# Kernel tuning notes

Hardware: AMD Instinct MI355X
Metric: run time of the kernel (lower is better)

The kernel has to match this reference:

```python
import jax, jax.numpy as jnp
import numpy as np

IN, HID, OUT, PHEAD = 128, 256, 256, 64
N0, E0, ND0, E1, ND1 = 1048576, 2097152, 131072, 131072, 8192

def setup_inputs() -> dict:
    key = jax.random.key(0)
    ks = jax.random.split(key, 12)
    x = jax.random.normal(ks[0], (N0, IN), dtype=jnp.float32)
    src0 = jax.random.randint(ks[1], (E0,), 0, N0)
    dst0 = jax.random.randint(ks[2], (E0,), 0, ND0)
    src1 = jax.random.randint(ks[3], (E1,), 0, ND0)
    dst1 = jax.random.randint(ks[4], (E1,), 0, ND1)
    s1 = 1.0 / np.sqrt(IN); s2 = 1.0 / np.sqrt(HID); s3 = 1.0 / np.sqrt(OUT)
    W1 = jax.random.uniform(ks[5], (HID, IN), jnp.float32, -s1, s1)
    b1 = jax.random.uniform(ks[6], (HID,), jnp.float32, -s1, s1)
    W2 = jax.random.uniform(ks[7], (OUT, HID), jnp.float32, -s2, s2)
    b2 = jax.random.uniform(ks[8], (OUT,), jnp.float32, -s2, s2)
    Wh = jax.random.uniform(ks[9], (PHEAD, OUT), jnp.float32, -s3, s3)
    bh = jax.random.uniform(ks[10], (PHEAD,), jnp.float32, -s3, s3)
    return {"x": x, "src0": src0, "dst0": dst0, "src1": src1, "dst1": dst1,
            "W1": W1, "b1": b1, "W2": W2, "b2": b2, "Wh": Wh, "bh": bh,
            "n_dst0": ND0, "n_dst1": ND1, "task_index": 0}

def sage_gcn(feat_src, feat_dst, src, dst, n_dst, W, b):
    # DGL SAGEConv aggregator_type='gcn': (sum_neighbors + self) / (deg + 1), then fc_neigh
    neigh = jax.ops.segment_sum(feat_src[src], dst, num_segments=n_dst)
    deg = jax.ops.segment_sum(jnp.ones((src.shape[0],), feat_src.dtype), dst, num_segments=n_dst)
    h = (neigh + feat_dst) / (deg + 1.0)[:, None]
    return h @ W.T + b

def reference(x, src0, dst0, src1, dst1, W1, b1, W2, b2, Wh, bh, n_dst0, n_dst1, task_index):
    h_dst = x[:n_dst0]
    h = jax.nn.relu(sage_gcn(x, h_dst, src0, dst0, n_dst0, W1, b1))
    h_dst = h[:n_dst1]
    h = jax.nn.relu(sage_gcn(h, h_dst, src1, dst1, n_dst1, W2, b2))
    if task_index == -1:
        return h
    return h @ Wh.T + bh
```

## Files before the change

kernel.cpp:

```cpp
#include <hip/hip_runtime.h>


#define GEMM_BM 64
#define GEMM_BN 64
#define GEMM_BK 32

__global__ __launch_bounds__(256) void hist_kernel(const int* __restrict__ dst,
                                                   int* __restrict__ count, int E) {
    int e = blockIdx.x * 256 + threadIdx.x;
    if (e >= E) return;
    atomicAdd(&count[dst[e]], 1);
}

__global__ __launch_bounds__(256) void block_sum_kernel(const int* __restrict__ count,
                                                        int* __restrict__ bsum) {
    __shared__ int sdata[256];
    int t = threadIdx.x;
    int i = blockIdx.x * 1024 + t * 4;
    int s = count[i] + count[i + 1] + count[i + 2] + count[i + 3];
    sdata[t] = s;
    __syncthreads();
    for (int off = 128; off > 0; off >>= 1) {
        if (t < off) sdata[t] += sdata[t + off];
        __syncthreads();
    }
    if (t == 0) bsum[blockIdx.x] = sdata[0];
}

__global__ __launch_bounds__(256) void scan_small_kernel(const int* __restrict__ bsum,
                                                         int* __restrict__ boff, int nb) {
    __shared__ int sdata[256];
    int t = threadIdx.x;
    int v = (t < nb) ? bsum[t] : 0;
    sdata[t] = v;
    __syncthreads();
    int val = v;
    for (int off = 1; off < 256; off <<= 1) {
        int x = (t >= off) ? sdata[t - off] : 0;
        __syncthreads();
        val += x;
        sdata[t] = val;
        __syncthreads();
    }
    if (t < nb) boff[t] = val - v;
}

__global__ __launch_bounds__(256) void scan_final_kernel(const int* __restrict__ count,
                                                         const int* __restrict__ boff,
                                                         int* __restrict__ row_start,
                                                         int* __restrict__ cursor) {
    __shared__ int sdata[256];
    int t = threadIdx.x;
    int base_i = blockIdx.x * 1024 + t * 4;
    int c0 = count[base_i], c1 = count[base_i + 1], c2 = count[base_i + 2], c3 = count[base_i + 3];
    int local = c0 + c1 + c2 + c3;
    sdata[t] = local;
    __syncthreads();
    int val = local;
    for (int off = 1; off < 256; off <<= 1) {
        int x = (t >= off) ? sdata[t - off] : 0;
        __syncthreads();
        val += x;
        sdata[t] = val;
        __syncthreads();
    }
    int base = boff[blockIdx.x] + (val - local);
    int r0 = base, r1 = r0 + c0, r2 = r1 + c1, r3 = r2 + c2;
    row_start[base_i] = r0; row_start[base_i + 1] = r1;
    row_start[base_i + 2] = r2; row_start[base_i + 3] = r3;
    cursor[base_i] = r0; cursor[base_i + 1] = r1;
    cursor[base_i + 2] = r2; cursor[base_i + 3] = r3;
}

__global__ __launch_bounds__(256) void fill_kernel(const int* __restrict__ src,
                                                   const int* __restrict__ dst,
                                                   int* __restrict__ cursor,
                                                   int* __restrict__ edge_src, int E) {
    int e = blockIdx.x * 256 + threadIdx.x;
    if (e >= E) return;
    int d = dst[e];
    int p = atomicAdd(&cursor[d], 1);
    edge_src[p] = src[e];
}

template<int RF> struct VecSel;
template<> struct VecSel<2> { using V = float2; };
template<> struct VecSel<4> { using V = float4; };

template<int RF>
__global__ __launch_bounds__(256) void agg_kernel(const float* __restrict__ feat,
                                                  const float* __restrict__ selff,
                                                  const int* __restrict__ row_start,
                                                  const int* __restrict__ count,
                                                  const int* __restrict__ edge_src,
                                                  float* __restrict__ neigh,
                                                  float* __restrict__ deg, int ND) {
    using V = typename VecSel<RF>::V;
    int w = (blockIdx.x * 256 + threadIdx.x) >> 6;
    int lane = threadIdx.x & 63;
    if (w >= ND) return;
    const int K = 64 * RF;
    size_t lo = (size_t)w * K + (size_t)lane * RF;
    V acc = *(const V*)(selff + lo);
    const int rs = row_start[w];
    const int cnt = count[w];

    for (int base = 0; base < cnt; base += 64) {
        const int rem = min(cnt - base, 64);
        const int idx = edge_src[rs + base + min(lane, rem - 1)];

        for (int jj = 0; jj < rem; jj += 8) {
            int s[8];
            float m[8];
            #pragma unroll
            for (int k = 0; k < 8; ++k) {
                int j = jj + k;
                s[k] = __shfl(idx, min(j, rem - 1));
                m[k] = (j < rem) ? 1.0f : 0.0f;
            }
            V v[8];
            #pragma unroll
            for (int k = 0; k < 8; ++k)
                v[k] = *(const V*)(feat + (size_t)s[k] * K + (size_t)lane * RF);
            #pragma unroll
            for (int k = 0; k < 8; ++k) {
                acc.x += v[k].x * m[k];
                acc.y += v[k].y * m[k];
                if constexpr (RF == 4) {
                    acc.z += v[k].z * m[k];
                    acc.w += v[k].w * m[k];
                }
            }
        }
    }
    *(V*)(neigh + lo) = acc;
    if (lane == 0) deg[w] = (float)(cnt + 1);
}

template<bool RELU, bool HAS_RS>
__global__ __launch_bounds__(256) void gemm_kernel(const float* __restrict__ A,
                                                   const float* __restrict__ deg,
                                                   const float* __restrict__ W,
                                                   const float* __restrict__ bias,
                                                   float* __restrict__ C,
                                                   int M, int N, int K) {
    __shared__ float As[GEMM_BK][GEMM_BM];
    __shared__ float Ws[GEMM_BK][GEMM_BN];

    const int t = threadIdx.x;
    const int row0 = blockIdx.x * GEMM_BM;
    const int col0 = blockIdx.y * GEMM_BN;

    const int tm = (t & 15) * 4;
    const int tn = (t >> 4) * 4;

    float acc[4][4] = {};

    const int lr = t >> 3;
    const int lk = (t & 7) * 4;

    for (int k0 = 0; k0 < K; k0 += GEMM_BK) {
        #pragma unroll
        for (int pass = 0; pass < 2; ++pass) {
            int r = lr + pass * 32;
            const float4 v = *(const float4*)(A + (size_t)(row0 + r) * K + k0 + lk);
            As[lk + 0][r] = v.x; As[lk + 1][r] = v.y;
            As[lk + 2][r] = v.z; As[lk + 3][r] = v.w;
        }
        #pragma unroll
        for (int pass = 0; pass < 2; ++pass) {
            int n = lr + pass * 32;
            const float4 v = *(const float4*)(W + (size_t)(col0 + n) * K + k0 + lk);
            Ws[lk + 0][n] = v.x; Ws[lk + 1][n] = v.y;
            Ws[lk + 2][n] = v.z; Ws[lk + 3][n] = v.w;
        }
        __syncthreads();

        #pragma unroll
        for (int k = 0; k < GEMM_BK; ++k) {
            const float4 a = *(const float4*)&As[k][tm];
            const float4 w = *(const float4*)&Ws[k][tn];
            acc[0][0] += a.x * w.x; acc[0][1] += a.x * w.y; acc[0][2] += a.x * w.z; acc[0][3] += a.x * w.w;
            acc[1][0] += a.y * w.x; acc[1][1] += a.y * w.y; acc[1][2] += a.y * w.z; acc[1][3] += a.y * w.w;
            acc[2][0] += a.z * w.x; acc[2][1] += a.z * w.y; acc[2][2] += a.z * w.z; acc[2][3] += a.z * w.w;
            acc[3][0] += a.w * w.x; acc[3][1] += a.w * w.y; acc[3][2] += a.w * w.z; acc[3][3] += a.w * w.w;
        }
        __syncthreads();
    }

    float scl[4];
    #pragma unroll
    for (int i = 0; i < 4; ++i)
        scl[i] = HAS_RS ? (1.0f / deg[row0 + tm + i]) : 1.0f;

    float bb[4];
    #pragma unroll
    for (int j = 0; j < 4; ++j) bb[j] = bias[col0 + tn + j];

    #pragma unroll
    for (int i = 0; i < 4; ++i) {
        float4 v;
        v.x = acc[i][0] * scl[i] + bb[0];
        v.y = acc[i][1] * scl[i] + bb[1];
        v.z = acc[i][2] * scl[i] + bb[2];
        v.w = acc[i][3] * scl[i] + bb[3];
        if (RELU) {
            v.x = fmaxf(v.x, 0.0f); v.y = fmaxf(v.y, 0.0f);
            v.z = fmaxf(v.z, 0.0f); v.w = fmaxf(v.w, 0.0f);
        }
        *(float4*)(C + (size_t)(row0 + tm + i) * N + col0 + tn) = v;
    }
}

extern "C" void kernel_launch(void* const* d_in, const int* in_sizes, int n_in,
                              void* d_out, int out_size, void* d_ws, size_t ws_size,
                              hipStream_t stream) {
    const float* x   = (const float*)d_in[0];
    const int* src0  = (const int*)d_in[1];
    const int* dst0  = (const int*)d_in[2];
    const int* src1  = (const int*)d_in[3];
    const int* dst1  = (const int*)d_in[4];
    const float* W1  = (const float*)d_in[5];
    const float* b1  = (const float*)d_in[6];
    const float* W2  = (const float*)d_in[7];
    const float* b2  = (const float*)d_in[8];
    const float* Wh  = (const float*)d_in[9];
    const float* bh  = (const float*)d_in[10];

    const int E0 = in_sizes[1];
    const int E1 = in_sizes[3];
    const int IN = 128, HID = 256, OUT = 256, PHEAD = 64;
    const int ND0 = 131072, ND1 = 8192;

    float* ws = (float*)d_ws;
    float* neigh0 = ws;
    float* deg0   = neigh0 + (size_t)ND0 * IN;
    float* h1     = deg0 + ND0;
    float* out    = (float*)d_out;

    int* count0     = (int*)h1;
    int* row_start0 = count0 + ND0;
    int* cursor0    = row_start0 + ND0;
    int* edge_src0  = cursor0 + ND0;
    int* bsum0      = edge_src0 + E0;
    int* boff0      = bsum0 + 256;

    float* neigh1 = neigh0;
    float* deg1   = neigh1 + (size_t)ND1 * HID;
    float* h2     = deg1 + ND1;
    int* count1     = (int*)(h2 + (size_t)ND1 * OUT);
    int* row_start1 = count1 + ND1;
    int* cursor1    = row_start1 + ND1;
    int* edge_src1  = cursor1 + ND1;
    int* bsum1      = edge_src1 + E1;
    int* boff1      = bsum1 + 256;

    hipMemsetAsync(count0, 0, ND0 * sizeof(int), stream);
    hist_kernel<<<E0 / 256, 256, 0, stream>>>(dst0, count0, E0);
    block_sum_kernel<<<ND0 / 1024, 256, 0, stream>>>(count0, bsum0);
    scan_small_kernel<<<1, 256, 0, stream>>>(bsum0, boff0, ND0 / 1024);
    scan_final_kernel<<<ND0 / 1024, 256, 0, stream>>>(count0, boff0, row_start0, cursor0);
    fill_kernel<<<E0 / 256, 256, 0, stream>>>(src0, dst0, cursor0, edge_src0, E0);
    agg_kernel<2><<<ND0 / 4, 256, 0, stream>>>(x, x, row_start0, count0, edge_src0,
                                               neigh0, deg0, ND0);
    {
        dim3 g(ND0 / GEMM_BM, HID / GEMM_BN);
        gemm_kernel<true, true><<<g, 256, 0, stream>>>(neigh0, deg0, W1, b1, h1, ND0, HID, IN);
    }

    hipMemsetAsync(count1, 0, ND1 * sizeof(int), stream);
    hist_kernel<<<E1 / 256, 256, 0, stream>>>(dst1, count1, E1);
    block_sum_kernel<<<ND1 / 1024, 256, 0, stream>>>(count1, bsum1);
    scan_small_kernel<<<1, 256, 0, stream>>>(bsum1, boff1, ND1 / 1024);
    scan_final_kernel<<<ND1 / 1024, 256, 0, stream>>>(count1, boff1, row_start1, cursor1);
    fill_kernel<<<E1 / 256, 256, 0, stream>>>(src1, dst1, cursor1, edge_src1, E1);
    agg_kernel<4><<<ND1 / 4, 256, 0, stream>>>(h1, h1, row_start1, count1, edge_src1,
                                               neigh1, deg1, ND1);
    {
        dim3 g(ND1 / GEMM_BM, OUT / GEMM_BN);
        gemm_kernel<true, true><<<g, 256, 0, stream>>>(neigh1, deg1, W2, b2, h2, ND1, OUT, HID);
    }

    {
        dim3 g(ND1 / GEMM_BM, PHEAD / GEMM_BN);
        gemm_kernel<false, false><<<g, 256, 0, stream>>>(h2, nullptr, Wh, bh, out, ND1, PHEAD, OUT);
    }
}
```

Measured before the change: 1.263 ms.

## Compute layer-one hidden rows only for nodes that layer two reads

Adds a pass that marks which layer-one destination nodes are actually read by layer two, either as self features (the first ND1 rows) or as sources in src1. A prefix scan over this mask gives each marked node a compact rank. The layer-one histogram, CSR fill, aggregation and GEMM then skip unmarked nodes and write compacted rows, and the layer-two CSR remaps its sources through the rank table. This cuts layer-one gather and GEMM work, at the cost of extra mark and scan kernels and one more indirection when building the layer-two CSR.

```diff
diff --git a/kernel.cpp b/kernel.cpp
--- a/kernel.cpp
+++ b/kernel.cpp
@@ -5,11 +5,23 @@
 #define GEMM_BN 64
 #define GEMM_BK 32
 
+__global__ __launch_bounds__(256) void mark_kernel(const int* __restrict__ src1,
+                                                   int* __restrict__ needed,
+                                                   int E, int nd1) {
+    int e = blockIdx.x * 256 + threadIdx.x;
+    if (e < nd1) needed[e] = 1;
+    if (e >= E) return;
+    needed[src1[e]] = 1;
+}
+
 __global__ __launch_bounds__(256) void hist_kernel(const int* __restrict__ dst,
+                                                   const int* __restrict__ needed,
                                                    int* __restrict__ count, int E) {
     int e = blockIdx.x * 256 + threadIdx.x;
     if (e >= E) return;
-    atomicAdd(&count[dst[e]], 1);
+    int d = dst[e];
+    if (needed != nullptr && needed[d] == 0) return;
+    atomicAdd(&count[d], 1);
 }
 
 __global__ __launch_bounds__(256) void block_sum_kernel(const int* __restrict__ count,
@@ -28,7 +40,8 @@
 }
 
 __global__ __launch_bounds__(256) void scan_small_kernel(const int* __restrict__ bsum,
-                                                         int* __restrict__ boff, int nb) {
+                                                         int* __restrict__ boff, int nb,
+                                                         int* __restrict__ total) {
     __shared__ int sdata[256];
     int t = threadIdx.x;
     int v = (t < nb) ? bsum[t] : 0;
@@ -43,6 +56,7 @@
         __syncthreads();
     }
     if (t < nb) boff[t] = val - v;
+    if (total != nullptr && t == nb - 1) *total = val;
 }
 
 __global__ __launch_bounds__(256) void scan_final_kernel(const int* __restrict__ count,
@@ -74,34 +88,47 @@
 
 __global__ __launch_bounds__(256) void fill_kernel(const int* __restrict__ src,
                                                    const int* __restrict__ dst,
+                                                   const int* __restrict__ needed,
+                                                   const int* __restrict__ remap,
                                                    int* __restrict__ cursor,
                                                    int* __restrict__ edge_src, int E) {
     int e = blockIdx.x * 256 + threadIdx.x;
     if (e >= E) return;
     int d = dst[e];
+    if (needed != nullptr && needed[d] == 0) return;
+    int s = src[e];
+    if (remap != nullptr) s = remap[s];
     int p = atomicAdd(&cursor[d], 1);
-    edge_src[p] = src[e];
+    edge_src[p] = s;
 }
 
 template<int RF> struct VecSel;
 template<> struct VecSel<2> { using V = float2; };
 template<> struct VecSel<4> { using V = float4; };
 
-template<int RF>
+template<int RF, bool COMPACT>
 __global__ __launch_bounds__(256) void agg_kernel(const float* __restrict__ feat,
                                                   const float* __restrict__ selff,
                                                   const int* __restrict__ row_start,
                                                   const int* __restrict__ count,
                                                   const int* __restrict__ edge_src,
+                                                  const int* __restrict__ needed,
+                                                  const int* __restrict__ rank,
                                                   float* __restrict__ neigh,
                                                   float* __restrict__ deg, int ND) {
     using V = typename VecSel<RF>::V;
     int w = (blockIdx.x * 256 + threadIdx.x) >> 6;
     int lane = threadIdx.x & 63;
     if (w >= ND) return;
+    int out_r = w;
+    if constexpr (COMPACT) {
+        if (needed[w] == 0) return;
+        out_r = rank[w];
+    }
     const int K = 64 * RF;
-    size_t lo = (size_t)w * K + (size_t)lane * RF;
-    V acc = *(const V*)(selff + lo);
+    size_t lo_in  = (size_t)w * K + (size_t)lane * RF;
+    size_t lo_out = (size_t)out_r * K + (size_t)lane * RF;
+    V acc = *(const V*)(selff + lo_in);
     const int rs = row_start[w];
     const int cnt = count[w];
 
@@ -133,22 +160,26 @@
             }
         }
     }
-    *(V*)(neigh + lo) = acc;
-    if (lane == 0) deg[w] = (float)(cnt + 1);
-}
-
-template<bool RELU, bool HAS_RS>
+    *(V*)(neigh + lo_out) = acc;
+    if (lane == 0) deg[out_r] = (float)(cnt + 1);
+}
+
+template<bool RELU, bool HAS_RS, bool DYNM>
 __global__ __launch_bounds__(256) void gemm_kernel(const float* __restrict__ A,
                                                    const float* __restrict__ deg,
                                                    const float* __restrict__ W,
                                                    const float* __restrict__ bias,
                                                    float* __restrict__ C,
-                                                   int M, int N, int K) {
+                                                   const int* __restrict__ m_ptr,
+                                                   int N, int K) {
     __shared__ float As[GEMM_BK][GEMM_BM];
     __shared__ float Ws[GEMM_BK][GEMM_BN];
 
     const int t = threadIdx.x;
     const int row0 = blockIdx.x * GEMM_BM;
+    if constexpr (DYNM) {
+        if (row0 >= *m_ptr) return;
+    }
     const int col0 = blockIdx.y * GEMM_BN;
 
     const int tm = (t & 15) * 4;
@@ -233,56 +264,68 @@
     const int ND0 = 131072, ND1 = 8192;
 
     float* ws = (float*)d_ws;
-    float* neigh0 = ws;
-    float* deg0   = neigh0 + (size_t)ND0 * IN;
-    float* h1     = deg0 + ND0;
-    float* out    = (float*)d_out;
-
-    int* count0     = (int*)h1;
-    int* row_start0 = count0 + ND0;
+    float* neigh0c = ws;
+    float* deg0c   = neigh0c + (size_t)ND0 * IN;
+    float* h1c     = deg0c + ND0;
+    float* neigh1  = h1c + (size_t)ND0 * HID;
+    float* deg1    = neigh1 + (size_t)ND1 * HID;
+    float* h2      = deg1 + ND1;
+    float* out     = (float*)d_out;
+
+    int* count0     = (int*)(h2 + (size_t)ND1 * OUT);
+    int* needed     = count0 + ND0;
+    int* count1     = needed + ND0;
+    int* rank       = count1 + ND1;
+    int* row_start0 = rank + ND0;
     int* cursor0    = row_start0 + ND0;
     int* edge_src0  = cursor0 + ND0;
-    int* bsum0      = edge_src0 + E0;
-    int* boff0      = bsum0 + 256;
-
-    float* neigh1 = neigh0;
-    float* deg1   = neigh1 + (size_t)ND1 * HID;
-    float* h2     = deg1 + ND1;
-    int* count1     = (int*)(h2 + (size_t)ND1 * OUT);
-    int* row_start1 = count1 + ND1;
+    int* row_start1 = edge_src0 + E0;
     int* cursor1    = row_start1 + ND1;
     int* edge_src1  = cursor1 + ND1;
-    int* bsum1      = edge_src1 + E1;
-    int* boff1      = bsum1 + 256;
-
-    hipMemsetAsync(count0, 0, ND0 * sizeof(int), stream);
-    hist_kernel<<<E0 / 256, 256, 0, stream>>>(dst0, count0, E0);
-    block_sum_kernel<<<ND0 / 1024, 256, 0, stream>>>(count0, bsum0);
-    scan_small_kernel<<<1, 256, 0, stream>>>(bsum0, boff0, ND0 / 1024);
-    scan_final_kernel<<<ND0 / 1024, 256, 0, stream>>>(count0, boff0, row_start0, cursor0);
-    fill_kernel<<<E0 / 256, 256, 0, stream>>>(src0, dst0, cursor0, edge_src0, E0);
-    agg_kernel<2><<<ND0 / 4, 256, 0, stream>>>(x, x, row_start0, count0, edge_src0,
-                                               neigh0, deg0, ND0);
+    int* bsumA      = edge_src1 + E1;
+    int* boffA      = bsumA + 256;
+    int* bsumB      = boffA + 256;
+    int* boffB      = bsumB + 256;
+    int* nr_ptr     = boffB + 256;
+
+    hipMemsetAsync(count0, 0, (size_t)(2 * ND0 + ND1) * sizeof(int), stream);
+
+    mark_kernel<<<E1 / 256, 256, 0, stream>>>(src1, needed, E1, ND1);
+    block_sum_kernel<<<ND0 / 1024, 256, 0, stream>>>(needed, bsumA);
+    scan_small_kernel<<<1, 256, 0, stream>>>(bsumA, boffA, ND0 / 1024, nr_ptr);
+    scan_final_kernel<<<ND0 / 1024, 256, 0, stream>>>(needed, boffA, rank, rank);
+
+    hist_kernel<<<E0 / 256, 256, 0, stream>>>(dst0, needed, count0, E0);
+    block_sum_kernel<<<ND0 / 1024, 256, 0, stream>>>(count0, bsumB);
+    scan_small_kernel<<<1, 256, 0, stream>>>(bsumB, boffB, ND0 / 1024, nullptr);
+    scan_final_kernel<<<ND0 / 1024, 256, 0, stream>>>(count0, boffB, row_start0, cursor0);
+    fill_kernel<<<E0 / 256, 256, 0, stream>>>(src0, dst0, needed, nullptr,
+                                              cursor0, edge_src0, E0);
+    agg_kernel<2, true><<<ND0 / 4, 256, 0, stream>>>(x, x, row_start0, count0, edge_src0,
+                                                     needed, rank, neigh0c, deg0c, ND0);
     {
         dim3 g(ND0 / GEMM_BM, HID / GEMM_BN);
-        gemm_kernel<true, true><<<g, 256, 0, stream>>>(neigh0, deg0, W1, b1, h1, ND0, HID, IN);
-    }
-
-    hipMemsetAsync(count1, 0, ND1 * sizeof(int), stream);
-    hist_kernel<<<E1 / 256, 256, 0, stream>>>(dst1, count1, E1);
-    block_sum_kernel<<<ND1 / 1024, 256, 0, stream>>>(count1, bsum1);
-    scan_small_kernel<<<1, 256, 0, stream>>>(bsum1, boff1, ND1 / 1024);
-    scan_final_kernel<<<ND1 / 1024, 256, 0, stream>>>(count1, boff1, row_start1, cursor1);
-    fill_kernel<<<E1 / 256, 256, 0, stream>>>(src1, dst1, cursor1, edge_src1, E1);
-    agg_kernel<4><<<ND1 / 4, 256, 0, stream>>>(h1, h1, row_start1, count1, edge_src1,
-                                               neigh1, deg1, ND1);
+        gemm_kernel<true, true, true><<<g, 256, 0, stream>>>(neigh0c, deg0c, W1, b1, h1c,
+                                                             nr_ptr, HID, IN);
+    }
+
+    hist_kernel<<<E1 / 256, 256, 0, stream>>>(dst1, nullptr, count1, E1);
+    block_sum_kernel<<<ND1 / 1024, 256, 0, stream>>>(count1, bsumB);
+    scan_small_kernel<<<1, 256, 0, stream>>>(bsumB, boffB, ND1 / 1024, nullptr);
+    scan_final_kernel<<<ND1 / 1024, 256, 0, stream>>>(count1, boffB, row_start1, cursor1);
+    fill_kernel<<<E1 / 256, 256, 0, stream>>>(src1, dst1, nullptr, rank,
+                                              cursor1, edge_src1, E1);
+    agg_kernel<4, false><<<ND1 / 4, 256, 0, stream>>>(h1c, h1c, row_start1, count1, edge_src1,
+                                                      nullptr, nullptr, neigh1, deg1, ND1);
     {
         dim3 g(ND1 / GEMM_BM, OUT / GEMM_BN);
-        gemm_kernel<true, true><<<g, 256, 0, stream>>>(neigh1, deg1, W2, b2, h2, ND1, OUT, HID);
+        gemm_kernel<true, true, false><<<g, 256, 0, stream>>>(neigh1, deg1, W2, b2, h2,
+                                                              nullptr, OUT, HID);
     }
 
     {
         dim3 g(ND1 / GEMM_BM, PHEAD / GEMM_BN);
-        gemm_kernel<false, false><<<g, 256, 0, stream>>>(h2, nullptr, Wh, bh, out, ND1, PHEAD, OUT);
-    }
-}
+        gemm_kernel<false, false, false><<<g, 256, 0, stream>>>(h2, nullptr, Wh, bh, out,
+                                                                nullptr, PHEAD, OUT);
+    }
+}
```

New measurement: 1.058 ms. 16.3% less time.
